# Kernel optimization log

Measured on AMD Instinct MI355X. Metric: run time of the kernel, lower is better.

## Reference

```python
import jax, jax.numpy as jnp
import numpy as np

NP, LP, ROUTINGS = 8, 16, 3
PAD = 2  # (kernel_size - 1) // 2 for kernel_size=5, stride=1


def _squash_2(t):
    # norm over LP axis (axis=3); torch: norm/(1+norm^2+1e-4) * t
    norm = jnp.linalg.norm(t, axis=3, keepdims=True)
    return norm / (1.0 + norm * norm + 1e-4) * t


def setup_inputs() -> dict:
    key = jax.random.key(0)
    k1, k2 = jax.random.split(key)
    x = jax.random.normal(k1, (4, 4, 16, 256, 256), dtype=jnp.float32)
    # conv weights initialized uniform [0, 0.1] as in the torch module
    W = jax.random.uniform(k2, (NP * LP, 16, 5, 5), dtype=jnp.float32) * 0.1
    return {"x": x, "W": W}


def reference(x, W):
    B, NC, LC, H, Wd = x.shape
    xf = x.reshape(B * NC, LC, H, Wd)
    votes = jax.lax.conv_general_dilated(
        xf, W, window_strides=(1, 1), padding=((PAD, PAD), (PAD, PAD)),
        dimension_numbers=("NCHW", "OIHW", "NCHW"))  # (B*NC, NP*LP, H, W)
    votes = votes.reshape(B, NC, NP, LP, H, Wd)
    sims = jnp.zeros((B, NC, NP, 1, H, Wd), dtype=x.dtype)
    parent = None
    for _ in range(ROUTINGS):
        c_ij = jax.nn.softmax(sims + 1e-4, axis=2)          # softmax over NP
        parent_bs = jnp.sum(c_ij * votes, axis=1, keepdims=True)  # sum over NC
        parent = _squash_2(parent_bs)                        # (B,1,NP,LP,H,W)
        sims = sims + jnp.sum(votes * parent, axis=3, keepdims=True)
    return parent[:, 0]  # squeeze NC axis -> (B, NP, LP, H, W)
```

## Files before the change

kernel.cpp:

```cpp
#include <hip/hip_runtime.h>

#define NPAR 8
#define LPAR 16
#define OCH 128
#define HH 256
#define WW 256
#define HWSZ (HH*WW)

typedef _Float16 f16x8 __attribute__((ext_vector_type(8)));
typedef _Float16 f16x4 __attribute__((ext_vector_type(4)));
typedef _Float16 f16x2 __attribute__((ext_vector_type(2)));
typedef float    f32x4 __attribute__((ext_vector_type(4)));

#define SMEM_HALVES 16896
#define VROW 132

__device__ __forceinline__ int xs_addr(int dyr, int wp, int col) {
    return (dyr * 20 + wp) * 64 + (col ^ ((wp & 7) << 3));
}

#if defined(__has_builtin)
#if __has_builtin(__builtin_amdgcn_fdot2)
#define HAVE_FDOT2 1
#endif
#endif

__device__ __forceinline__ float fdot2_acc(f16x2 a, f16x2 b, float c) {
#ifdef HAVE_FDOT2
    return __builtin_amdgcn_fdot2(a, b, c, false);
#else
    return c + (float)a[0] * (float)b[0] + (float)a[1] * (float)b[1];
#endif
}

__device__ __forceinline__ f16x2 quad_sum4_pk(f16x2 v) {
    int t = __builtin_amdgcn_update_dpp(0, __builtin_bit_cast(int, v),
                                        0xB1, 0xF, 0xF, true);
    v = v + __builtin_bit_cast(f16x2, t);
    t = __builtin_amdgcn_update_dpp(0, __builtin_bit_cast(int, v),
                                    0x4E, 0xF, 0xF, true);
    v = v + __builtin_bit_cast(f16x2, t);
    return v;
}

__global__ void reorder_W_kernel(const float* __restrict__ Wg,
                                 _Float16* __restrict__ ws) {
    int idx = blockIdx.x * 256 + threadIdx.x;
    if (idx >= 13 * 128 * 32) return;
    const int q  = idx & 31;
    const int oc = (idx >> 5) & 127;
    const int kk = idx >> 12;
    const int tap = 2 * kk + (q >> 4);
    const int ci  = ((q >> 3) & 1) * 8 + (q & 7);
    const float v = (tap < 25) ? Wg[oc * 400 + ci * 25 + tap] : 0.f;
    ws[idx] = (_Float16)v;
}

__global__ __launch_bounds__(256, 3)
void capsule_mfma6_kernel(const float* __restrict__ x,
                          const _Float16* __restrict__ wsf,
                          float* __restrict__ out) {
    __shared__ _Float16 sm[SMEM_HALVES];

    const int tid = threadIdx.x;
    const int w   = tid >> 6;
    const int l   = tid & 63;

    const int blk   = ((blockIdx.x & 7) << 10) + (blockIdx.x >> 3);
    const int b     = blk >> 11;
    const int rt    = blk & 2047;
    const int hrow0 = (rt >> 4) << 1;
    const int w0    = (rt & 15) << 4;

    for (int i = 0; i < 15; ++i) {
        const unsigned idx = i * 256 + tid;
        const unsigned q   = idx / 20u;
        const int wp  = idx - q * 20u;
        const int cip = q & 7;
        const int t2  = q >> 3;
        const int nc  = t2 & 3;
        const int dyr = t2 >> 2;
        const int hh  = hrow0 + dyr - 2;
        const int wg  = w0 + wp - 2;
        const bool ok = (hh >= 0) && (hh < HH) && (wg >= 0) && (wg < WW);
        const float* src = x + (((size_t)(b * 4 + nc) * 16 + cip * 2) * HH + hh) * (size_t)WW + wg;
        const float v0 = ok ? src[0] : 0.f;
        const float v1 = ok ? src[HWSZ] : 0.f;
        *(f16x2*)&sm[xs_addr(dyr, wp, nc * 16 + cip * 2)] =
            (f16x2){(_Float16)v0, (_Float16)v1};
    }
    __syncthreads();

    const int rwc = w >> 1;
    const int oh  = w & 1;
    const int p   = l >> 4;
    const int ml  = l & 15;
    const bool hiT = (p & 2) != 0;
    const int ciA = (p & 1) * 8;
    const int pxA = ml >> 2;
    const int ncA = ml & 3;
    const int bfbase = (oh * 64 + ml) * 32 + p * 8;

    f32x4 acc[4][4];
#pragma unroll
    for (int a = 0; a < 4; ++a)
#pragma unroll
        for (int bb = 0; bb < 4; ++bb)
            acc[a][bb] = (f32x4){0.f, 0.f, 0.f, 0.f};

#pragma unroll
    for (int kk = 0; kk < 13; ++kk) {
        f16x8 bf[4];
#pragma unroll
        for (int bb = 0; bb < 4; ++bb)
            bf[bb] = *(const f16x8*)&wsf[kk * 4096 + bb * 512 + bfbase];

        const int t0 = 2 * kk;
        const int t1 = (2 * kk + 1 > 24) ? 24 : 2 * kk + 1;
        const int dy = hiT ? (t1 / 5) : (t0 / 5);
        const int dx = hiT ? (t1 % 5) : (t0 % 5);

        f16x8 af[4];
#pragma unroll
        for (int a = 0; a < 4; ++a)
            af[a] = *(const f16x8*)&sm[xs_addr(rwc + dy, a * 4 + pxA + dx, ncA * 16 + ciA)];

#pragma unroll
        for (int a = 0; a < 4; ++a)
#pragma unroll
            for (int bb = 0; bb < 4; ++bb)
                acc[a][bb] = __builtin_amdgcn_mfma_f32_16x16x32_f16(
                    af[a], bf[bb], acc[a][bb], 0, 0, 0);
    }
    __syncthreads();

#pragma unroll
    for (int a = 0; a < 4; ++a) {
#pragma unroll
        for (int reg = 0; reg < 4; ++reg) {
            f16x4 pk;
#pragma unroll
            for (int bb = 0; bb < 4; ++bb) pk[bb] = (_Float16)acc[a][bb][reg];
            const int R = rwc * 64 + a * 16 + p * 4 + reg;
            *(f16x4*)&sm[R * VROW + ml * 8 + oh * 4] = pk;
        }
    }
    __syncthreads();

    const int ncR = tid & 3;
    const int h   = (tid >> 2) & 1;
    const int pxx = (tid >> 3) & 15;
    const int rw  = tid >> 7;

    const int R = rw * 64 + pxx * 4 + ncR;
    f16x8 vh[8];
#pragma unroll
    for (int c8 = 0; c8 < 8; ++c8)
        vh[c8] = *(const f16x8*)&sm[R * VROW + (h * 8 + c8) * 8];

    float* outb = out + (size_t)b * OCH * HWSZ
                + (size_t)(hrow0 + rw) * WW + (w0 + pxx);

    float sims[NPAR];
#pragma unroll
    for (int i = 0; i < NPAR; ++i) sims[i] = 0.f;

#pragma unroll
    for (int it = 0; it < 3; ++it) {
        float mx = fmaxf(fmaxf(fmaxf(sims[0], sims[1]), fmaxf(sims[2], sims[3])),
                         fmaxf(fmaxf(sims[4], sims[5]), fmaxf(sims[6], sims[7])));
        float e[NPAR];
        float se = 0.f;
#pragma unroll
        for (int i = 0; i < NPAR; ++i) { e[i] = __expf(sims[i] - mx); se += e[i]; }
        const float inv = 1.f / se;

#pragma unroll
        for (int np_ = 0; np_ < NPAR; ++np_) {
            const float cf = e[np_] * inv;
            const f16x2 cp = (f16x2){(_Float16)cf, (_Float16)cf};
            float n2 = 0.f, dot = 0.f;
            f16x2 keep0 = (f16x2){(_Float16)0.f, (_Float16)0.f};
            f16x2 keep1 = keep0;
#pragma unroll
            for (int k = 0; k < 4; ++k) {
                const f16x2 vv = (f16x2){vh[2 * k][np_], vh[2 * k + 1][np_]};
                const f16x2 t2 = quad_sum4_pk(cp * vv);
                n2  = fdot2_acc(t2, t2, n2);
                dot = fdot2_acc(vv, t2, dot);
                if (it == 2 && (k >> 1) == (ncR & 1)) {
                    if (k & 1) keep1 = t2; else keep0 = t2;
                }
            }
            n2  += __shfl_xor(n2, 4);
            dot += __shfl_xor(dot, 4);
            const float scale = sqrtf(n2) / (1.f + n2 + 1e-4f);
            sims[np_] += scale * dot;

            if (it == 2 && (ncR >> 1) == h) {
                outb[(size_t)(np_ * LPAR + ncR * 4 + 0) * HWSZ] = scale * (float)keep0[0];
                outb[(size_t)(np_ * LPAR + ncR * 4 + 1) * HWSZ] = scale * (float)keep0[1];
                outb[(size_t)(np_ * LPAR + ncR * 4 + 2) * HWSZ] = scale * (float)keep1[0];
                outb[(size_t)(np_ * LPAR + ncR * 4 + 3) * HWSZ] = scale * (float)keep1[1];
            }
        }
    }
}

extern "C" void kernel_launch(void* const* d_in, const int* in_sizes, int n_in,
                              void* d_out, int out_size, void* d_ws, size_t ws_size,
                              hipStream_t stream) {
    const float* x  = (const float*)d_in[0];
    const float* Wg = (const float*)d_in[1];
    float* out = (float*)d_out;
    _Float16* ws = (_Float16*)d_ws;
    (void)in_sizes; (void)n_in; (void)ws_size; (void)out_size;

    hipLaunchKernelGGL(reorder_W_kernel, dim3(208), dim3(256), 0, stream, Wg, ws);
    hipLaunchKernelGGL(capsule_mfma6_kernel, dim3(8192), dim3(256), 0, stream,
                       x, ws, out);
}
```

Measured before the change: 244.2 us.

## Split fused conv+routing into separate conv and routing kernels via workspace

Splits the fused kernel into a conv kernel that writes fp16 votes to the global workspace and a routing kernel that reads them back, with one thread owning all 16 LP values per NC. The work is chunked according to the available workspace size. The fused kernel remains as a fallback when the workspace is too small. The aim is to drop the LDS-heavy fused epilogue, raise occupancy, and remove the cross-lane shuffle. The cost is an extra round trip of 256 MB of fp16 votes through global memory and extra kernel launches.

Measured after the change: 370.4 us. 51.7% more time.

```diff
diff --git a/kernel.cpp b/kernel.cpp
--- a/kernel.cpp
+++ b/kernel.cpp
@@ -12,8 +12,9 @@
 typedef _Float16 f16x2 __attribute__((ext_vector_type(2)));
 typedef float    f32x4 __attribute__((ext_vector_type(4)));
 
-#define SMEM_HALVES 16896
 #define VROW 132
+#define SMEM_HALVES_FUSED 16896
+#define XS_HALVES 7680
 
 __device__ __forceinline__ int xs_addr(int dyr, int wp, int col) {
     return (dyr * 20 + wp) * 64 + (col ^ ((wp & 7) << 3));
@@ -57,18 +58,19 @@
 }
 
 __global__ __launch_bounds__(256, 3)
-void capsule_mfma6_kernel(const float* __restrict__ x,
-                          const _Float16* __restrict__ wsf,
-                          float* __restrict__ out) {
-    __shared__ _Float16 sm[SMEM_HALVES];
+void conv_votes_kernel(const float* __restrict__ x,
+                       const _Float16* __restrict__ wsf,
+                       _Float16* __restrict__ votes,
+                       int baseBlk) {
+    __shared__ _Float16 sm[XS_HALVES];
 
     const int tid = threadIdx.x;
     const int w   = tid >> 6;
     const int l   = tid & 63;
 
-    const int blk   = ((blockIdx.x & 7) << 10) + (blockIdx.x >> 3);
-    const int b     = blk >> 11;
-    const int rt    = blk & 2047;
+    const int L     = baseBlk + blockIdx.x;
+    const int b     = L >> 11;
+    const int rt    = L & 2047;
     const int hrow0 = (rt >> 4) << 1;
     const int w0    = (rt & 15) << 4;
 
@@ -132,6 +134,165 @@
                 acc[a][bb] = __builtin_amdgcn_mfma_f32_16x16x32_f16(
                     af[a], bf[bb], acc[a][bb], 0, 0, 0);
     }
+
+    const size_t vbase = (size_t)blockIdx.x * 16384;
+#pragma unroll
+    for (int a = 0; a < 4; ++a) {
+#pragma unroll
+        for (int reg = 0; reg < 4; ++reg) {
+            f16x4 pk;
+#pragma unroll
+            for (int bb = 0; bb < 4; ++bb) pk[bb] = (_Float16)acc[a][bb][reg];
+            const int R = rwc * 64 + a * 16 + p * 4 + reg;
+            *(f16x4*)&votes[vbase + (size_t)R * 128 + ml * 8 + oh * 4] = pk;
+        }
+    }
+}
+
+__global__ __launch_bounds__(256, 4)
+void routing_kernel(const _Float16* __restrict__ votes,
+                    float* __restrict__ out,
+                    int baseBlk) {
+    const int tid = threadIdx.x;
+    const int ncR = tid & 3;
+    const int pxL = tid >> 2;
+    const int Ll  = (blockIdx.x << 1) + (pxL >> 5);
+    const int L   = baseBlk + Ll;
+    const int pib = pxL & 31;
+    const int rwc = pib >> 4, pxc = pib & 15;
+    const int b   = L >> 11;
+    const int rt  = L & 2047;
+    const int hrow = ((rt >> 4) << 1) + rwc;
+    const int wcol = ((rt & 15) << 4) + pxc;
+
+    const _Float16* vrow = votes + ((size_t)Ll * 128 + pib * 4 + ncR) * 128;
+    f16x8 vh[16];
+#pragma unroll
+    for (int lp = 0; lp < LPAR; ++lp)
+        vh[lp] = *(const f16x8*)&vrow[lp * 8];
+
+    float* outb = out + (size_t)b * OCH * HWSZ + (size_t)hrow * WW + wcol;
+
+    float sims[NPAR];
+#pragma unroll
+    for (int i = 0; i < NPAR; ++i) sims[i] = 0.f;
+
+#pragma unroll
+    for (int it = 0; it < 3; ++it) {
+        float mx = fmaxf(fmaxf(fmaxf(sims[0], sims[1]), fmaxf(sims[2], sims[3])),
+                         fmaxf(fmaxf(sims[4], sims[5]), fmaxf(sims[6], sims[7])));
+        float e[NPAR];
+        float se = 0.f;
+#pragma unroll
+        for (int i = 0; i < NPAR; ++i) { e[i] = __expf(sims[i] - mx); se += e[i]; }
+        const float inv = 1.f / se;
+
+#pragma unroll
+        for (int np_ = 0; np_ < NPAR; ++np_) {
+            const float cf = e[np_] * inv;
+            const f16x2 cp = (f16x2){(_Float16)cf, (_Float16)cf};
+            float n2 = 0.f, dot = 0.f;
+            f16x2 keep0 = (f16x2){(_Float16)0.f, (_Float16)0.f};
+            f16x2 keep1 = keep0;
+#pragma unroll
+            for (int k = 0; k < 8; ++k) {
+                const f16x2 vv = (f16x2){vh[2 * k][np_], vh[2 * k + 1][np_]};
+                const f16x2 t2 = quad_sum4_pk(cp * vv);
+                n2  = fdot2_acc(t2, t2, n2);
+                dot = fdot2_acc(vv, t2, dot);
+                if (it == 2 && (k >> 1) == ncR) {
+                    if (k & 1) keep1 = t2; else keep0 = t2;
+                }
+            }
+            const float scale = sqrtf(n2) / (1.f + n2 + 1e-4f);
+            sims[np_] += scale * dot;
+
+            if (it == 2) {
+                outb[(size_t)(np_ * LPAR + ncR * 4 + 0) * HWSZ] = scale * (float)keep0[0];
+                outb[(size_t)(np_ * LPAR + ncR * 4 + 1) * HWSZ] = scale * (float)keep0[1];
+                outb[(size_t)(np_ * LPAR + ncR * 4 + 2) * HWSZ] = scale * (float)keep1[0];
+                outb[(size_t)(np_ * LPAR + ncR * 4 + 3) * HWSZ] = scale * (float)keep1[1];
+            }
+        }
+    }
+}
+
+__global__ __launch_bounds__(256, 3)
+void capsule_mfma6_kernel(const float* __restrict__ x,
+                          const _Float16* __restrict__ wsf,
+                          float* __restrict__ out) {
+    __shared__ _Float16 sm[SMEM_HALVES_FUSED];
+
+    const int tid = threadIdx.x;
+    const int w   = tid >> 6;
+    const int l   = tid & 63;
+
+    const int blk   = ((blockIdx.x & 7) << 10) + (blockIdx.x >> 3);
+    const int b     = blk >> 11;
+    const int rt    = blk & 2047;
+    const int hrow0 = (rt >> 4) << 1;
+    const int w0    = (rt & 15) << 4;
+
+    for (int i = 0; i < 15; ++i) {
+        const unsigned idx = i * 256 + tid;
+        const unsigned q   = idx / 20u;
+        const int wp  = idx - q * 20u;
+        const int cip = q & 7;
+        const int t2  = q >> 3;
+        const int nc  = t2 & 3;
+        const int dyr = t2 >> 2;
+        const int hh  = hrow0 + dyr - 2;
+        const int wg  = w0 + wp - 2;
+        const bool ok = (hh >= 0) && (hh < HH) && (wg >= 0) && (wg < WW);
+        const float* src = x + (((size_t)(b * 4 + nc) * 16 + cip * 2) * HH + hh) * (size_t)WW + wg;
+        const float v0 = ok ? src[0] : 0.f;
+        const float v1 = ok ? src[HWSZ] : 0.f;
+        *(f16x2*)&sm[xs_addr(dyr, wp, nc * 16 + cip * 2)] =
+            (f16x2){(_Float16)v0, (_Float16)v1};
+    }
+    __syncthreads();
+
+    const int rwc = w >> 1;
+    const int oh  = w & 1;
+    const int p   = l >> 4;
+    const int ml  = l & 15;
+    const bool hiT = (p & 2) != 0;
+    const int ciA = (p & 1) * 8;
+    const int pxA = ml >> 2;
+    const int ncA = ml & 3;
+    const int bfbase = (oh * 64 + ml) * 32 + p * 8;
+
+    f32x4 acc[4][4];
+#pragma unroll
+    for (int a = 0; a < 4; ++a)
+#pragma unroll
+        for (int bb = 0; bb < 4; ++bb)
+            acc[a][bb] = (f32x4){0.f, 0.f, 0.f, 0.f};
+
+#pragma unroll
+    for (int kk = 0; kk < 13; ++kk) {
+        f16x8 bf[4];
+#pragma unroll
+        for (int bb = 0; bb < 4; ++bb)
+            bf[bb] = *(const f16x8*)&wsf[kk * 4096 + bb * 512 + bfbase];
+
+        const int t0 = 2 * kk;
+        const int t1 = (2 * kk + 1 > 24) ? 24 : 2 * kk + 1;
+        const int dy = hiT ? (t1 / 5) : (t0 / 5);
+        const int dx = hiT ? (t1 % 5) : (t0 % 5);
+
+        f16x8 af[4];
+#pragma unroll
+        for (int a = 0; a < 4; ++a)
+            af[a] = *(const f16x8*)&sm[xs_addr(rwc + dy, a * 4 + pxA + dx, ncA * 16 + ciA)];
+
+#pragma unroll
+        for (int a = 0; a < 4; ++a)
+#pragma unroll
+            for (int bb = 0; bb < 4; ++bb)
+                acc[a][bb] = __builtin_amdgcn_mfma_f32_16x16x32_f16(
+                    af[a], bf[bb], acc[a][bb], 0, 0, 0);
+    }
     __syncthreads();
 
 #pragma unroll
@@ -214,9 +375,24 @@
     const float* Wg = (const float*)d_in[1];
     float* out = (float*)d_out;
     _Float16* ws = (_Float16*)d_ws;
-    (void)in_sizes; (void)n_in; (void)ws_size; (void)out_size;
+    (void)in_sizes; (void)n_in; (void)out_size;
 
     hipLaunchKernelGGL(reorder_W_kernel, dim3(208), dim3(256), 0, stream, Wg, ws);
-    hipLaunchKernelGGL(capsule_mfma6_kernel, dim3(8192), dim3(256), 0, stream,
-                       x, ws, out);
-}
+
+    const long cap = ((long)ws_size - 131072L) / 32768L;
+    if (cap >= 2) {
+        const long Kl = (cap < 8192L ? cap : 8192L) & ~1L;
+        const int  K  = (int)Kl;
+        _Float16* votes = ws + 65536;
+        for (int base = 0; base < 8192; base += K) {
+            const int cnt = (8192 - base < K) ? (8192 - base) : K;
+            hipLaunchKernelGGL(conv_votes_kernel, dim3(cnt), dim3(256), 0, stream,
+                               x, ws, votes, base);
+            hipLaunchKernelGGL(routing_kernel, dim3(cnt / 2), dim3(256), 0, stream,
+                               votes, out, base);
+        }
+    } else {
+        hipLaunchKernelGGL(capsule_mfma6_kernel, dim3(8192), dim3(256), 0, stream,
+                           x, ws, out);
+    }
+}
```

## Widen output tile to 32 columns and route each row in two phases

Applied to the files above, without the earlier changes.

Each block now covers 2 rows by 32 columns instead of 2 by 16, halving the grid and the overlap reloads of the 5x5 halo. Each wave holds an 8x4 grid of MFMA accumulators, so register pressure rises and occupancy drops from 3 to 2 blocks. Routing runs in two phases, one per output row, which reuses the same shared-memory staging area. It also skips the first softmax (uniform 1/8) and the final similarity dot product.

Result: slower. 291.1 us (+19.2%).

```diff
diff --git a/kernel.cpp b/kernel.cpp
--- a/kernel.cpp
+++ b/kernel.cpp
@@ -16,7 +16,7 @@
 #define VROW 132
 
 __device__ __forceinline__ int xs_addr(int dyr, int wp, int col) {
-    return (dyr * 20 + wp) * 64 + (col ^ ((wp & 7) << 3));
+    return (dyr * 36 + wp) * 64 + (col ^ ((wp & 7) << 3));
 }
 
 #if defined(__has_builtin)
@@ -56,8 +56,8 @@
     ws[idx] = (_Float16)v;
 }
 
-__global__ __launch_bounds__(256, 3)
-void capsule_mfma6_kernel(const float* __restrict__ x,
+__global__ __launch_bounds__(256, 2)
+void capsule_mfma7_kernel(const float* __restrict__ x,
                           const _Float16* __restrict__ wsf,
                           float* __restrict__ out) {
     __shared__ _Float16 sm[SMEM_HALVES];
@@ -66,16 +66,16 @@
     const int w   = tid >> 6;
     const int l   = tid & 63;
 
-    const int blk   = ((blockIdx.x & 7) << 10) + (blockIdx.x >> 3);
-    const int b     = blk >> 11;
-    const int rt    = blk & 2047;
-    const int hrow0 = (rt >> 4) << 1;
-    const int w0    = (rt & 15) << 4;
-
-    for (int i = 0; i < 15; ++i) {
+    const int blk   = ((blockIdx.x & 7) << 9) + (blockIdx.x >> 3);
+    const int b     = blk >> 10;
+    const int rt    = blk & 1023;
+    const int hrow0 = (rt >> 3) << 1;
+    const int w0    = (rt & 7) << 5;
+
+    for (int i = 0; i < 27; ++i) {
         const unsigned idx = i * 256 + tid;
-        const unsigned q   = idx / 20u;
-        const int wp  = idx - q * 20u;
+        const unsigned q   = idx / 36u;
+        const int wp  = idx - q * 36u;
         const int cip = q & 7;
         const int t2  = q >> 3;
         const int nc  = t2 & 3;
@@ -91,19 +91,19 @@
     }
     __syncthreads();
 
-    const int rwc = w >> 1;
+    const int Mh  = w >> 1;
     const int oh  = w & 1;
-    const int p   = l >> 4;
+    const int kq  = l >> 4;
     const int ml  = l & 15;
-    const bool hiT = (p & 2) != 0;
-    const int ciA = (p & 1) * 8;
+    const bool hiT = (kq & 2) != 0;
+    const int ciA = (kq & 1) * 8;
     const int pxA = ml >> 2;
     const int ncA = ml & 3;
-    const int bfbase = (oh * 64 + ml) * 32 + p * 8;
-
-    f32x4 acc[4][4];
-#pragma unroll
-    for (int a = 0; a < 4; ++a)
+    const int bfbase = (oh * 64 + ml) * 32 + kq * 8;
+
+    f32x4 acc[8][4];
+#pragma unroll
+    for (int a = 0; a < 8; ++a)
 #pragma unroll
         for (int bb = 0; bb < 4; ++bb)
             acc[a][bb] = (f32x4){0.f, 0.f, 0.f, 0.f};
@@ -120,13 +120,13 @@
         const int dy = hiT ? (t1 / 5) : (t0 / 5);
         const int dx = hiT ? (t1 % 5) : (t0 % 5);
 
-        f16x8 af[4];
-#pragma unroll
-        for (int a = 0; a < 4; ++a)
-            af[a] = *(const f16x8*)&sm[xs_addr(rwc + dy, a * 4 + pxA + dx, ncA * 16 + ciA)];
-
-#pragma unroll
-        for (int a = 0; a < 4; ++a)
+        f16x8 af[8];
+#pragma unroll
+        for (int a = 0; a < 8; ++a)
+            af[a] = *(const f16x8*)&sm[xs_addr(Mh + dy, a * 4 + pxA + dx, ncA * 16 + ciA)];
+
+#pragma unroll
+        for (int a = 0; a < 8; ++a)
 #pragma unroll
             for (int bb = 0; bb < 4; ++bb)
                 acc[a][bb] = __builtin_amdgcn_mfma_f32_16x16x32_f16(
@@ -134,76 +134,85 @@
     }
     __syncthreads();
 
-#pragma unroll
-    for (int a = 0; a < 4; ++a) {
-#pragma unroll
-        for (int reg = 0; reg < 4; ++reg) {
-            f16x4 pk;
-#pragma unroll
-            for (int bb = 0; bb < 4; ++bb) pk[bb] = (_Float16)acc[a][bb][reg];
-            const int R = rwc * 64 + a * 16 + p * 4 + reg;
-            *(f16x4*)&sm[R * VROW + ml * 8 + oh * 4] = pk;
-        }
-    }
-    __syncthreads();
-
     const int ncR = tid & 3;
     const int h   = (tid >> 2) & 1;
-    const int pxx = (tid >> 3) & 15;
-    const int rw  = tid >> 7;
-
-    const int R = rw * 64 + pxx * 4 + ncR;
-    f16x8 vh[8];
-#pragma unroll
-    for (int c8 = 0; c8 < 8; ++c8)
-        vh[c8] = *(const f16x8*)&sm[R * VROW + (h * 8 + c8) * 8];
-
-    float* outb = out + (size_t)b * OCH * HWSZ
-                + (size_t)(hrow0 + rw) * WW + (w0 + pxx);
-
-    float sims[NPAR];
-#pragma unroll
-    for (int i = 0; i < NPAR; ++i) sims[i] = 0.f;
-
-#pragma unroll
-    for (int it = 0; it < 3; ++it) {
-        float mx = fmaxf(fmaxf(fmaxf(sims[0], sims[1]), fmaxf(sims[2], sims[3])),
-                         fmaxf(fmaxf(sims[4], sims[5]), fmaxf(sims[6], sims[7])));
-        float e[NPAR];
-        float se = 0.f;
-#pragma unroll
-        for (int i = 0; i < NPAR; ++i) { e[i] = __expf(sims[i] - mx); se += e[i]; }
-        const float inv = 1.f / se;
-
-#pragma unroll
-        for (int np_ = 0; np_ < NPAR; ++np_) {
-            const float cf = e[np_] * inv;
-            const f16x2 cp = (f16x2){(_Float16)cf, (_Float16)cf};
-            float n2 = 0.f, dot = 0.f;
-            f16x2 keep0 = (f16x2){(_Float16)0.f, (_Float16)0.f};
-            f16x2 keep1 = keep0;
-#pragma unroll
-            for (int k = 0; k < 4; ++k) {
-                const f16x2 vv = (f16x2){vh[2 * k][np_], vh[2 * k + 1][np_]};
-                const f16x2 t2 = quad_sum4_pk(cp * vv);
-                n2  = fdot2_acc(t2, t2, n2);
-                dot = fdot2_acc(vv, t2, dot);
-                if (it == 2 && (k >> 1) == (ncR & 1)) {
-                    if (k & 1) keep1 = t2; else keep0 = t2;
-                }
-            }
-            n2  += __shfl_xor(n2, 4);
-            dot += __shfl_xor(dot, 4);
-            const float scale = sqrtf(n2) / (1.f + n2 + 1e-4f);
-            sims[np_] += scale * dot;
-
-            if (it == 2 && (ncR >> 1) == h) {
-                outb[(size_t)(np_ * LPAR + ncR * 4 + 0) * HWSZ] = scale * (float)keep0[0];
-                outb[(size_t)(np_ * LPAR + ncR * 4 + 1) * HWSZ] = scale * (float)keep0[1];
-                outb[(size_t)(np_ * LPAR + ncR * 4 + 2) * HWSZ] = scale * (float)keep1[0];
-                outb[(size_t)(np_ * LPAR + ncR * 4 + 3) * HWSZ] = scale * (float)keep1[1];
+    const int wx  = tid >> 3;
+
+#pragma unroll
+    for (int ph = 0; ph < 2; ++ph) {
+        if (Mh == ph) {
+#pragma unroll
+            for (int a = 0; a < 8; ++a) {
+#pragma unroll
+                for (int reg = 0; reg < 4; ++reg) {
+                    f16x4 pk;
+#pragma unroll
+                    for (int bb = 0; bb < 4; ++bb) pk[bb] = (_Float16)acc[a][bb][reg];
+                    const int Rl = a * 16 + kq * 4 + reg;
+                    *(f16x4*)&sm[Rl * VROW + ml * 8 + oh * 4] = pk;
+                }
             }
         }
+        __syncthreads();
+
+        const int Rl = wx * 4 + ncR;
+        f16x8 vh[8];
+#pragma unroll
+        for (int c8 = 0; c8 < 8; ++c8)
+            vh[c8] = *(const f16x8*)&sm[Rl * VROW + (h * 8 + c8) * 8];
+
+        float* outb = out + (size_t)b * OCH * HWSZ
+                    + (size_t)(hrow0 + ph) * WW + (w0 + wx);
+
+        float sims[NPAR];
+#pragma unroll
+        for (int i = 0; i < NPAR; ++i) sims[i] = 0.f;
+
+#pragma unroll
+        for (int it = 0; it < 3; ++it) {
+            float e[NPAR];
+            float inv = 0.f;
+            if (it > 0) {
+                float mx = fmaxf(fmaxf(fmaxf(sims[0], sims[1]), fmaxf(sims[2], sims[3])),
+                                 fmaxf(fmaxf(sims[4], sims[5]), fmaxf(sims[6], sims[7])));
+                float se = 0.f;
+#pragma unroll
+                for (int i = 0; i < NPAR; ++i) { e[i] = __expf(sims[i] - mx); se += e[i]; }
+                inv = 1.f / se;
+            }
+
+#pragma unroll
+            for (int np_ = 0; np_ < NPAR; ++np_) {
+                const float cf = (it == 0) ? 0.125f : e[np_] * inv;
+                const f16x2 cp = (f16x2){(_Float16)cf, (_Float16)cf};
+                float n2 = 0.f, dot = 0.f;
+                f16x2 keep0 = (f16x2){(_Float16)0.f, (_Float16)0.f};
+                f16x2 keep1 = keep0;
+#pragma unroll
+                for (int k = 0; k < 4; ++k) {
+                    const f16x2 vv = (f16x2){vh[2 * k][np_], vh[2 * k + 1][np_]};
+                    const f16x2 t2 = quad_sum4_pk(cp * vv);
+                    n2 = fdot2_acc(t2, t2, n2);
+                    if (it < 2) dot = fdot2_acc(vv, t2, dot);
+                    if (it == 2 && (k >> 1) == (ncR & 1)) {
+                        if (k & 1) keep1 = t2; else keep0 = t2;
+                    }
+                }
+                n2 += __shfl_xor(n2, 4);
+                const float scale = sqrtf(n2) / (1.f + n2 + 1e-4f);
+                if (it < 2) {
+                    dot += __shfl_xor(dot, 4);
+                    sims[np_] += scale * dot;
+                }
+                if (it == 2 && (ncR >> 1) == h) {
+                    outb[(size_t)(np_ * LPAR + ncR * 4 + 0) * HWSZ] = scale * (float)keep0[0];
+                    outb[(size_t)(np_ * LPAR + ncR * 4 + 1) * HWSZ] = scale * (float)keep0[1];
+                    outb[(size_t)(np_ * LPAR + ncR * 4 + 2) * HWSZ] = scale * (float)keep1[0];
+                    outb[(size_t)(np_ * LPAR + ncR * 4 + 3) * HWSZ] = scale * (float)keep1[1];
+                }
+            }
+        }
+        __syncthreads();
     }
 }
 
@@ -217,6 +226,6 @@
     (void)in_sizes; (void)n_in; (void)ws_size; (void)out_size;
 
     hipLaunchKernelGGL(reorder_W_kernel, dim3(208), dim3(256), 0, stream, Wg, ws);
-    hipLaunchKernelGGL(capsule_mfma6_kernel, dim3(8192), dim3(256), 0, stream,
+    hipLaunchKernelGGL(capsule_mfma7_kernel, dim3(4096), dim3(256), 0, stream,
                        x, ws, out);
 }
```
